# Kernel optimization log

Measured on AMD Instinct MI355X. Metric: run time of the kernel, lower is better.

Reference implementation:

```python
import jax, jax.numpy as jnp
import numpy as np


def setup_inputs() -> dict:
    key = jax.random.key(0)
    vel = jax.random.normal(key, (10000, 1000, 3), dtype=jnp.float32)
    return {"vel": vel, "vacf_window": 100}


def reference(vel, vacf_window):
    # vel: [T, N, 3]; output: [vacf_window]
    T = vel.shape[0]
    flat = vel.reshape(T, -1)  # [T, N*3]
    # lag 0: mean(vel * vel)
    terms = [jnp.mean(flat * flat)]
    # lags 1..vacf_window-1: mean over (T - t) * N * 3 elements
    for t in range(1, vacf_window):
        terms.append(jnp.mean(flat[t:] * flat[:-t]))
    return jnp.stack(terms)
```

## Files before the change

### kernel.cpp

```cpp
#include <hip/hip_runtime.h>


#define T_DIM 10000
#define C_DIM 3000
#define W 100

#define CHUNKS 96
#define RPAD 10368
#define GRAN 64
#define PITCH 576
#define YOFF 4096
#define WS_NEED (YOFF + (size_t)CHUNKS * RPAD * GRAN)

#define MA 256
#define NA 16
#define SROWS 384
#define NBB 40
#define KSPLIT 16
#define CPB 6
#define TILEB (SROWS * GRAN)
#define NPART 8

#define FB_MA 112
#define FB_NA 7
#define FB_SROWS 224
#define FB_NBB 90
#define FB_KSPLIT 24
#define FB_CPB 4
#define FB_KB 32
#define FB_LPAD 34

typedef __attribute__((ext_vector_type(8))) short short8;
typedef __attribute__((ext_vector_type(4))) short short4v;
typedef __attribute__((ext_vector_type(4))) float float4v;
typedef __attribute__((ext_vector_type(4))) unsigned int uint4v;

__device__ __forceinline__ short f2bf(float f) {
    unsigned u = __float_as_uint(f);
    u += 0x7fffu + ((u >> 16) & 1u);
    return (short)(u >> 16);
}

__device__ __forceinline__ void gload_lds16(const char* src, char* dst) {
    __builtin_amdgcn_global_load_lds(
        (const __attribute__((address_space(1))) unsigned int*)src,
        (__attribute__((address_space(3))) unsigned int*)dst, 16, 0, 0);
}

__global__ __launch_bounds__(256)
void vacf_relayout(const float* __restrict__ X, char* __restrict__ Y) {
    __shared__ __align__(16) char tile[64 * PITCH];
    const int tid = threadIdx.x;
    const int l   = tid & 63;
    const int w   = tid >> 6;
    const int bc  = blockIdx.x % 12;
    const int br  = blockIdx.x / 12;
    const int r0  = br * 64;
    const int c0  = bc * 256;

    #pragma unroll
    for (int k = 0; k < 16; ++k) {
        const int rl  = k * 4 + w;
        const int col = l * 4;
        const int row = r0 + rl;
        float4v v = {0.f, 0.f, 0.f, 0.f};
        if (row < T_DIM && c0 + col + 4 <= C_DIM)
            v = *(const float4v*)(X + (size_t)row * C_DIM + c0 + col);
        short4v o;
        o[0] = f2bf(v[0]); o[1] = f2bf(v[1]); o[2] = f2bf(v[2]); o[3] = f2bf(v[3]);
        const int cc = col >> 5, p = (col >> 3) & 3, sub = col & 7;
        const int ps = p ^ ((rl >> 1) & 3);
        *(short4v*)&tile[rl * PITCH + cc * 64 + ps * 16 + sub * 2] = o;
    }
    __syncthreads();

    const int rl = 16 * w + (l >> 2);
    const int q  = l & 3;
    const char* s = &tile[rl * PITCH + q * 16];
    #pragma unroll
    for (int cc = 0; cc < 8; ++cc) {
        char* dst = Y + ((size_t)(bc * 8 + cc) * RPAD + r0 + rl) * GRAN + q * 16;
        *(uint4v*)dst = *(const uint4v*)(s + cc * 64);
    }
}

__global__ __launch_bounds__(256, 3)
void vacf_main(const char* __restrict__ Y, float* __restrict__ partial) {
    const int tid  = threadIdx.x;
    const int lane = tid & 63;
    const int wv   = tid >> 6;
    const int xcd  = blockIdx.x & 7;
    const int j    = blockIdx.x >> 3;
    const int ksix = xcd + 8 * (j / NBB);
    const int bb   = j % NBB;
    const int i0   = bb * MA;

    __shared__ __align__(16) char lds[2 * TILEB];
    __shared__ float bins[W];
    if (tid < W) bins[tid] = 0.f;

    const int n    = lane & 15;
    const int quad = lane >> 4;
    const int d0   = 2 * wv;
    const int fragoff = n * 64 + ((quad ^ ((n >> 1) & 3)) << 4);
    const int lr16 = lane * 16;

    float4v acc0 = {0.f, 0.f, 0.f, 0.f};
    float4v acc1 = {0.f, 0.f, 0.f, 0.f};

    #define STAGE(bi, cix)                                                     \
        {                                                                      \
            const char* sb = Y + ((size_t)(cix) * RPAD + i0 + wv * 96) * GRAN; \
            char* db = lds + (bi) * TILEB + wv * 96 * GRAN;                    \
            _Pragma("unroll")                                                  \
            for (int m = 0; m < 6; ++m)                                        \
                gload_lds16(sb + m * 1024 + lr16, db + m * 1024);              \
        }

    STAGE(0, ksix * CPB)

    #pragma unroll
    for (int it = 0; it < CPB; ++it) {
        const int cur = it & 1;
        if (it + 1 < CPB) {
            STAGE(cur ^ 1, ksix * CPB + it + 1)
            asm volatile("s_waitcnt vmcnt(6)" ::: "memory");
        } else {
            asm volatile("s_waitcnt vmcnt(0)" ::: "memory");
        }
        __builtin_amdgcn_s_barrier();

        const char* lb = lds + cur * TILEB + fragoff;
        short8 fbp = *(const short8*)(lb + d0 * 1024);
        #pragma unroll
        for (int a = 0; a < NA; ++a) {
            const short8 fav = *(const short8*)(lb + a * 1024);
            const short8 fbn = *(const short8*)(lb + (d0 + a + 1) * 1024);
            acc0 = __builtin_amdgcn_mfma_f32_16x16x32_bf16(fav, fbp, acc0, 0, 0, 0);
            acc1 = __builtin_amdgcn_mfma_f32_16x16x32_bf16(fav, fbn, acc1, 0, 0, 0);
            fbp = fbn;
        }

        __builtin_amdgcn_sched_barrier(0);
        __builtin_amdgcn_s_barrier();
    }
    #undef STAGE

    #pragma unroll
    for (int p = 0; p < 4; ++p) {
        const int m  = quad * 4 + p;
        const int t0 = 16 * d0 + n - m;
        if (t0 >= 0 && t0 < W) atomicAdd(&bins[t0], acc0[p]);
        const int t1 = t0 + 16;
        if (t1 >= 0 && t1 < W) atomicAdd(&bins[t1], acc1[p]);
    }
    __syncthreads();
    if (tid < W) atomicAdd(&partial[xcd * W + tid], bins[tid]);
}

__global__ __launch_bounds__(256, 2)
void vacf_fb(const float* __restrict__ X, float* __restrict__ partial) {
    const int tid  = threadIdx.x;
    const int lane = tid & 63;
    const int wv   = tid >> 6;
    const int xcd  = blockIdx.x & 7;
    const int j    = blockIdx.x >> 3;
    const int ksix = xcd + 8 * (j / FB_NBB);
    const int bb   = j % FB_NBB;
    const int i0   = bb * FB_MA;
    const int ks   = ksix * (FB_CPB * FB_KB);
    const int ke   = (ks + FB_CPB * FB_KB < C_DIM) ? (ks + FB_CPB * FB_KB) : C_DIM;
    const int nit  = (ke - ks + FB_KB - 1) / FB_KB;

    __shared__ short buf[FB_SROWS * FB_LPAD];
    __shared__ float bins[W];
    if (tid < W) bins[tid] = 0.f;

    const int cp = tid & 7;
    const int r0 = tid >> 3;
    const int n    = lane & 15;
    const int quad = lane >> 4;
    const int d0   = 2 * wv;
    const short* fragbase = &buf[n * FB_LPAD + quad * 8];

    float4v acc0 = {0.f, 0.f, 0.f, 0.f};
    float4v acc1 = {0.f, 0.f, 0.f, 0.f};
    float4v pf[FB_NA];

    {
        #pragma unroll
        for (int s = 0; s < FB_NA; ++s) {
            const int row = i0 + r0 + 32 * s;
            const int col = ks + 4 * cp;
            pf[s] = (row < T_DIM) ? *(const float4v*)(X + (size_t)row * C_DIM + col)
                                  : (float4v){0.f, 0.f, 0.f, 0.f};
        }
    }

    #pragma unroll 1
    for (int it = 0; it < nit; ++it) {
        __syncthreads();
        #pragma unroll
        for (int s = 0; s < FB_NA; ++s) {
            short4v o;
            o[0] = f2bf(pf[s][0]); o[1] = f2bf(pf[s][1]);
            o[2] = f2bf(pf[s][2]); o[3] = f2bf(pf[s][3]);
            *(short4v*)&buf[(r0 + 32 * s) * FB_LPAD + 4 * cp] = o;
        }
        __syncthreads();

        if (it + 1 < nit) {
            const int k0 = ks + (it + 1) * FB_KB;
            const bool kfull = (k0 + FB_KB <= ke);
            #pragma unroll
            for (int s = 0; s < FB_NA; ++s) {
                const int row = i0 + r0 + 32 * s;
                const int col = k0 + 4 * cp;
                if ((row < T_DIM) & kfull) {
                    pf[s] = *(const float4v*)(X + (size_t)row * C_DIM + col);
                } else {
                    #pragma unroll
                    for (int e = 0; e < 4; ++e)
                        pf[s][e] = (row < T_DIM && col + e < ke)
                                     ? X[(size_t)row * C_DIM + col + e] : 0.f;
                }
            }
        }

        short8 fa[FB_NA], fb[8];
        #pragma unroll
        for (int a = 0; a < FB_NA; ++a)
            fa[a] = *(const short8*)(fragbase + 16 * a * FB_LPAD);
        #pragma unroll
        for (int u = 0; u < 8; ++u)
            fb[u] = *(const short8*)(fragbase + 16 * (d0 + u) * FB_LPAD);

        #pragma unroll
        for (int a = 0; a < FB_NA; ++a) {
            acc0 = __builtin_amdgcn_mfma_f32_16x16x32_bf16(fa[a], fb[a],     acc0, 0, 0, 0);
            acc1 = __builtin_amdgcn_mfma_f32_16x16x32_bf16(fa[a], fb[a + 1], acc1, 0, 0, 0);
        }
    }

    #pragma unroll
    for (int p = 0; p < 4; ++p) {
        const int m  = quad * 4 + p;
        const int t0 = 16 * d0 + n - m;
        if (t0 >= 0 && t0 < W) atomicAdd(&bins[t0], acc0[p]);
        const int t1 = t0 + 16;
        if (t1 >= 0 && t1 < W) atomicAdd(&bins[t1], acc1[p]);
    }
    __syncthreads();
    if (tid < W) atomicAdd(&partial[xcd * W + tid], bins[tid]);
}

__global__ void vacf_scale(const float* __restrict__ partial, float* __restrict__ out) {
    int t = threadIdx.x;
    if (t < W) {
        float s = 0.f;
        #pragma unroll
        for (int b = 0; b < NPART; ++b) s += partial[b * W + t];
        out[t] = s / ((float)(T_DIM - t) * (float)C_DIM);
    }
}

extern "C" void kernel_launch(void* const* d_in, const int* in_sizes, int n_in,
                              void* d_out, int out_size, void* d_ws, size_t ws_size,
                              hipStream_t stream) {
    const float* X = (const float*)d_in[0];
    float* out = (float*)d_out;
    float* ws  = (float*)d_ws;

    hipMemsetAsync(ws, 0, NPART * W * sizeof(float), stream);
    if (ws_size >= WS_NEED) {
        char* Y = (char*)d_ws + YOFF;
        vacf_relayout<<<(RPAD / 64) * 12, 256, 0, stream>>>(X, Y);
        vacf_main<<<NBB * KSPLIT, 256, 0, stream>>>(Y, ws);
    } else {
        vacf_fb<<<FB_NBB * FB_KSPLIT, 256, 0, stream>>>(X, ws);
    }
    vacf_scale<<<1, 128, 0, stream>>>(ws, out);
}
```

Measured before the change: 203.6 us.

## Load all chunks upfront in vacf_main with doubled k-split, nontemporal relayout loads

The main kernel now doubles the k-split count and halves chunks per block, loading all three chunk tiles into LDS in one burst with a single wait and barrier instead of a double-buffered per-chunk pipeline. This removes the per-iteration barriers and waits, doubles the grid for more parallelism, and lowers occupancy to two blocks per CU because of the larger LDS footprint. The relayout kernel gains an interior fast path with nontemporal float4 loads and no bounds checks. The cost is twice as many atomic partial adds and no overlap between loading and MFMA work within a block.

```diff
diff --git a/kernel.cpp b/kernel.cpp
--- a/kernel.cpp
+++ b/kernel.cpp
@@ -16,9 +16,9 @@
 #define NA 16
 #define SROWS 384
 #define NBB 40
-#define KSPLIT 16
-#define CPB 6
-#define TILEB (SROWS * GRAN)
+#define KSPLIT 32
+#define CPB 3
+#define CTILE (SROWS * GRAN)
 #define NPART 8
 
 #define FB_MA 112
@@ -45,6 +45,10 @@
     __builtin_amdgcn_global_load_lds(
         (const __attribute__((address_space(1))) unsigned int*)src,
         (__attribute__((address_space(3))) unsigned int*)dst, 16, 0, 0);
+}
+
+__device__ __forceinline__ float4v ntload4(const float* p) {
+    return __builtin_nontemporal_load((const float4v*)p);
 }
 
 __global__ __launch_bounds__(256)
@@ -58,19 +62,34 @@
     const int r0  = br * 64;
     const int c0  = bc * 256;
 
-    #pragma unroll
-    for (int k = 0; k < 16; ++k) {
-        const int rl  = k * 4 + w;
-        const int col = l * 4;
-        const int row = r0 + rl;
-        float4v v = {0.f, 0.f, 0.f, 0.f};
-        if (row < T_DIM && c0 + col + 4 <= C_DIM)
-            v = *(const float4v*)(X + (size_t)row * C_DIM + c0 + col);
-        short4v o;
-        o[0] = f2bf(v[0]); o[1] = f2bf(v[1]); o[2] = f2bf(v[2]); o[3] = f2bf(v[3]);
-        const int cc = col >> 5, p = (col >> 3) & 3, sub = col & 7;
-        const int ps = p ^ ((rl >> 1) & 3);
-        *(short4v*)&tile[rl * PITCH + cc * 64 + ps * 16 + sub * 2] = o;
+    const bool interior = (r0 + 64 <= T_DIM) && (c0 + 256 <= C_DIM);
+    if (interior) {
+        #pragma unroll
+        for (int k = 0; k < 16; ++k) {
+            const int rl  = k * 4 + w;
+            const int col = l * 4;
+            const float4v v = ntload4(X + (size_t)(r0 + rl) * C_DIM + c0 + col);
+            short4v o;
+            o[0] = f2bf(v[0]); o[1] = f2bf(v[1]); o[2] = f2bf(v[2]); o[3] = f2bf(v[3]);
+            const int cc = col >> 5, p = (col >> 3) & 3, sub = col & 7;
+            const int ps = p ^ ((rl >> 1) & 3);
+            *(short4v*)&tile[rl * PITCH + cc * 64 + ps * 16 + sub * 2] = o;
+        }
+    } else {
+        #pragma unroll
+        for (int k = 0; k < 16; ++k) {
+            const int rl  = k * 4 + w;
+            const int col = l * 4;
+            const int row = r0 + rl;
+            float4v v = {0.f, 0.f, 0.f, 0.f};
+            if (row < T_DIM && c0 + col + 4 <= C_DIM)
+                v = *(const float4v*)(X + (size_t)row * C_DIM + c0 + col);
+            short4v o;
+            o[0] = f2bf(v[0]); o[1] = f2bf(v[1]); o[2] = f2bf(v[2]); o[3] = f2bf(v[3]);
+            const int cc = col >> 5, p = (col >> 3) & 3, sub = col & 7;
+            const int ps = p ^ ((rl >> 1) & 3);
+            *(short4v*)&tile[rl * PITCH + cc * 64 + ps * 16 + sub * 2] = o;
+        }
     }
     __syncthreads();
 
@@ -84,7 +103,7 @@
     }
 }
 
-__global__ __launch_bounds__(256, 3)
+__global__ __launch_bounds__(256, 2)
 void vacf_main(const char* __restrict__ Y, float* __restrict__ partial) {
     const int tid  = threadIdx.x;
     const int lane = tid & 63;
@@ -95,7 +114,7 @@
     const int bb   = j % NBB;
     const int i0   = bb * MA;
 
-    __shared__ __align__(16) char lds[2 * TILEB];
+    __shared__ __align__(16) char lds[CPB * CTILE];
     __shared__ float bins[W];
     if (tid < W) bins[tid] = 0.f;
 
@@ -105,32 +124,23 @@
     const int fragoff = n * 64 + ((quad ^ ((n >> 1) & 3)) << 4);
     const int lr16 = lane * 16;
 
+    #pragma unroll
+    for (int cc = 0; cc < CPB; ++cc) {
+        const char* sb = Y + ((size_t)(ksix * CPB + cc) * RPAD + i0 + wv * 96) * GRAN;
+        char* db = lds + cc * CTILE + wv * 96 * GRAN;
+        #pragma unroll
+        for (int m = 0; m < 6; ++m)
+            gload_lds16(sb + m * 1024 + lr16, db + m * 1024);
+    }
+    asm volatile("s_waitcnt vmcnt(0)" ::: "memory");
+    __builtin_amdgcn_s_barrier();
+
     float4v acc0 = {0.f, 0.f, 0.f, 0.f};
     float4v acc1 = {0.f, 0.f, 0.f, 0.f};
 
-    #define STAGE(bi, cix)                                                     \
-        {                                                                      \
-            const char* sb = Y + ((size_t)(cix) * RPAD + i0 + wv * 96) * GRAN; \
-            char* db = lds + (bi) * TILEB + wv * 96 * GRAN;                    \
-            _Pragma("unroll")                                                  \
-            for (int m = 0; m < 6; ++m)                                        \
-                gload_lds16(sb + m * 1024 + lr16, db + m * 1024);              \
-        }
-
-    STAGE(0, ksix * CPB)
-
-    #pragma unroll
-    for (int it = 0; it < CPB; ++it) {
-        const int cur = it & 1;
-        if (it + 1 < CPB) {
-            STAGE(cur ^ 1, ksix * CPB + it + 1)
-            asm volatile("s_waitcnt vmcnt(6)" ::: "memory");
-        } else {
-            asm volatile("s_waitcnt vmcnt(0)" ::: "memory");
-        }
-        __builtin_amdgcn_s_barrier();
-
-        const char* lb = lds + cur * TILEB + fragoff;
+    #pragma unroll
+    for (int cc = 0; cc < CPB; ++cc) {
+        const char* lb = lds + cc * CTILE + fragoff;
         short8 fbp = *(const short8*)(lb + d0 * 1024);
         #pragma unroll
         for (int a = 0; a < NA; ++a) {
@@ -140,11 +150,7 @@
             acc1 = __builtin_amdgcn_mfma_f32_16x16x32_bf16(fav, fbn, acc1, 0, 0, 0);
             fbp = fbn;
         }
-
-        __builtin_amdgcn_sched_barrier(0);
-        __builtin_amdgcn_s_barrier();
-    }
-    #undef STAGE
+    }
 
     #pragma unroll
     for (int p = 0; p < 4; ++p) {
```

Result: slower. 208.0 us (+2.1%).
